# Optimization experiments

Measured on AMD Instinct MI355X. Metric: run time of the kernel, lower is better.

## Reference

```python
import jax, jax.numpy as jnp
import numpy as np

GROUPS = 32
EPS = 1e-5


def conv1x1(x, w, b):
    # x: [B,C,T], w: [O,C], b: [O]
    return jnp.einsum('bct,oc->bot', x, w) + b[None, :, None]


def group_norm(x, g, be):
    B, C, T = x.shape
    xg = x.reshape(B, GROUPS, C // GROUPS, T)
    mean = xg.mean(axis=(2, 3), keepdims=True)
    var = xg.var(axis=(2, 3), keepdims=True)
    xg = (xg - mean) * jax.lax.rsqrt(var + EPS)
    return xg.reshape(B, C, T) * g[None, :, None] + be[None, :, None]


def block(x, w, b, g, be):
    return jax.nn.relu(group_norm(conv1x1(x, w, b), g, be))


def _build_table(x, L):
    # sparse table for range-max: tabs[k][..., t] = max(x[..., t : t+2^k]) (clamped)
    T = x.shape[-1]
    tabs = [x]
    for k in range(1, L + 1):
        step = 1 << (k - 1)
        idx = jnp.minimum(jnp.arange(T) + step, T - 1)
        tabs.append(jnp.maximum(tabs[-1], tabs[-1][..., idx]))
    return jnp.stack(tabs)  # [L+1, B, C, T]


def _range_max_query(S, s, e):
    # S: [L+1,B,C,T]; s,e: [B,N] inclusive range -> [B,C,N]
    length = jnp.maximum(e - s + 1, 1)
    k = jnp.floor(jnp.log2(length.astype(jnp.float32))).astype(jnp.int32)
    e2 = jnp.maximum(e - jnp.left_shift(1, k) + 1, 0)

    def per_b(Sb, kb, sb, eb):
        # Sb: [L+1,C,T]; returns [N,C]
        return jnp.maximum(Sb[kb, :, sb], Sb[kb, :, eb])

    out = jax.vmap(per_b, in_axes=(1, 0, 0, 0))(S, k, s, e2)  # [B,N,C]
    return out.transpose(0, 2, 1)


def boundary_max_pooling(x, segments):
    # x: [B,C,T]; segments: [B,N,4] float boundaries -> [B,C,N]
    B, C, T = x.shape
    s = jnp.clip(jnp.floor(segments).astype(jnp.int32), 0, T - 1)
    e = jnp.clip(jnp.ceil(segments).astype(jnp.int32), 0, T - 1)
    L = max(1, int(np.ceil(np.log2(T))))
    half = C // 2
    S = _build_table(x, L)
    left = _range_max_query(S[:, :, :half], s[..., 0], jnp.maximum(e[..., 1], s[..., 0]))
    right = _range_max_query(S[:, :, half:], s[..., 2], jnp.maximum(e[..., 3], s[..., 2]))
    return jnp.concatenate([left, right], axis=1)


def setup_inputs() -> dict:
    key = jax.random.key(0)
    ks = jax.random.split(key, 12)
    B, Cin, pc, T, Tf, N = 4, 512, 256, 2048, 4096, 2048
    f = lambda k, sh: jax.random.normal(k, sh, jnp.float32)

    def segs(k, tmax):
        raw = jax.random.uniform(k, (B, N, 4), jnp.float32, 0.0, tmax - 1.0)
        return jnp.concatenate([jnp.sort(raw[..., :2], -1), jnp.sort(raw[..., 2:], -1)], -1)

    return {
        'feature': f(ks[0], (B, Cin, T)),
        'frame_level_feature': f(ks[1], (B, pc, Tf)),
        'segments': segs(ks[2], T),
        'frame_segments': segs(ks[3], Tf),
        'feature_lastclass': f(ks[4], (B, 250, N)),
        'ConfResult_feature': f(ks[5], (B, 250, N)),
        'w_cur': f(ks[6], (pc, Cin)) * 0.02, 'b_cur': jnp.zeros((pc,)),
        'g_cur': jnp.ones((pc,)), 'be_cur': jnp.zeros((pc,)),
        'w_lr': f(ks[7], (2 * pc, Cin)) * 0.02, 'b_lr': jnp.zeros((2 * pc,)),
        'g_lr': jnp.ones((2 * pc,)), 'be_lr': jnp.zeros((2 * pc,)),
        'w_roi': f(ks[8], (pc, pc)) * 0.02, 'b_roi': jnp.zeros((pc,)),
        'g_roi': jnp.ones((pc,)), 'be_roi': jnp.zeros((pc,)),
        'w_prop': f(ks[9], (Cin, 4 * pc + 500)) * 0.02, 'b_prop': jnp.zeros((Cin,)),
        'g_prop': jnp.ones((Cin,)), 'be_prop': jnp.zeros((Cin,)),
    }


def reference(feature, frame_level_feature, segments, frame_segments,
              feature_lastclass, ConfResult_feature,
              w_cur, b_cur, g_cur, be_cur,
              w_lr, b_lr, g_lr, be_lr,
              w_roi, b_roi, g_roi, be_roi,
              w_prop, b_prop, g_prop, be_prop):
    fm_short = block(feature, w_cur, b_cur, g_cur, be_cur)          # [B,pc,T]
    feat = block(feature, w_lr, b_lr, g_lr, be_lr)                  # [B,2pc,T]
    prop_feature = boundary_max_pooling(feat, segments)             # [B,2pc,N]
    prop_roi = boundary_max_pooling(frame_level_feature, frame_segments)  # [B,pc,N]
    prop_roi = block(prop_roi, w_roi, b_roi, g_roi, be_roi)
    cat = jnp.concatenate([prop_roi, prop_feature, fm_short,
                           feature_lastclass, ConfResult_feature], axis=1)  # [B,4pc+500,N]
    out = block(cat, w_prop, b_prop, g_prop, be_prop)               # [B,Cin,N]
    return (out, feat)
```

## Files before the change

### kernel.cpp

```cpp
#include <hip/hip_runtime.h>
#include <hip/hip_bf16.h>

#define GROUPS 32
#define EPS_GN 1e-5f

typedef short bf16x8 __attribute__((ext_vector_type(8)));
typedef float f32x4 __attribute__((ext_vector_type(4)));

__device__ __forceinline__ ushort to_bf16_bits(float v) {
  __hip_bfloat16 h = __float2bfloat16(v);
  return *(ushort*)&h;
}
__device__ __forceinline__ float bflo(unsigned u) { return __uint_as_float(u << 16); }
__device__ __forceinline__ float bfhi(unsigned u) { return __uint_as_float(u & 0xffff0000u); }
__device__ __forceinline__ ushort bfpack(float f) {
  return (ushort)(__float_as_uint(f) >> 16);
}

__global__ __launch_bounds__(256)
void cast_w_kernel(const float* __restrict__ w, ushort* __restrict__ wb,
                   int K, int Kp, int total)
{
  int idx = blockIdx.x * 256 + threadIdx.x;
  if (idx >= total) return;
  int o = idx / Kp, k = idx - o * Kp;
  float v = (k < K) ? w[(size_t)o * K + k] : 0.f;
  wb[idx] = to_bf16_bits(v);
}

__global__ __launch_bounds__(256)
void transpose_cast_off(const float* __restrict__ src, ushort* __restrict__ dst,
                        int C, int T, int dstride, int coff, int Cpad)
{
  __shared__ float tile[32][33];
  const int b = blockIdx.z;
  const int c0 = blockIdx.y * 32, t0 = blockIdx.x * 32;
  const int tx = threadIdx.x & 31, ty = threadIdx.x >> 5;
#pragma unroll
  for (int i = 0; i < 4; ++i) {
    const int c = c0 + ty + 8 * i;
    tile[ty + 8 * i][tx] = (c < C) ? src[((size_t)b * C + c) * T + t0 + tx] : 0.f;
  }
  __syncthreads();
  const int cw = c0 + tx;
  if (cw >= Cpad) return;
#pragma unroll
  for (int i = 0; i < 4; ++i)
    dst[((size_t)b * T + t0 + ty + 8 * i) * dstride + coff + cw] =
        to_bf16_bits(tile[tx][ty + 8 * i]);
}

__global__ __launch_bounds__(256)
void bmx_reduce(const ushort* __restrict__ src, ushort* __restrict__ dst,
                int C, int rows, int total8)
{
  int idx = blockIdx.x * 256 + threadIdx.x;
  if (idx >= total8) return;
  const int nc8 = C >> 3;
  const int ci = idx % nc8;
  const int rt = idx / nc8;
  const ushort* p = src + (size_t)rt * rows * C + ci * 8;
  float m[8];
#pragma unroll
  for (int i = 0; i < 8; ++i) m[i] = -3.402823466e38f;
  for (int j = 0; j < rows; ++j) {
    const uint4 v = *(const uint4*)(p + (size_t)j * C);
    m[0] = fmaxf(m[0], bflo(v.x)); m[1] = fmaxf(m[1], bfhi(v.x));
    m[2] = fmaxf(m[2], bflo(v.y)); m[3] = fmaxf(m[3], bfhi(v.y));
    m[4] = fmaxf(m[4], bflo(v.z)); m[5] = fmaxf(m[5], bfhi(v.z));
    m[6] = fmaxf(m[6], bflo(v.w)); m[7] = fmaxf(m[7], bfhi(v.w));
  }
  uint4 o;
  o.x = (unsigned)bfpack(m[0]) | ((unsigned)bfpack(m[1]) << 16);
  o.y = (unsigned)bfpack(m[2]) | ((unsigned)bfpack(m[3]) << 16);
  o.z = (unsigned)bfpack(m[4]) | ((unsigned)bfpack(m[5]) << 16);
  o.w = (unsigned)bfpack(m[6]) | ((unsigned)bfpack(m[7]) << 16);
  *(uint4*)(dst + (size_t)rt * C + ci * 8) = o;
}

template<int CHL>
__global__ __launch_bounds__(256)
void pool_t_kernel(const ushort* __restrict__ xt, const ushort* __restrict__ bx32,
                   const ushort* __restrict__ bx8, const float* __restrict__ segs,
                   ushort* __restrict__ dst,
                   int C, int T, int TB32, int TB8, int N, int dstride, int coff)
{
  const int b    = blockIdx.z;
  const int half = blockIdx.y;
  const int n    = blockIdx.x * 4 + (threadIdx.x >> 6);
  const int lane = threadIdx.x & 63;
  const int c    = half * (C >> 1) + lane * CHL;

  const float4 sg = *(const float4*)(segs + ((size_t)b * N + n) * 4);
  const float f0 = half ? sg.z : sg.x;
  const float f1 = half ? sg.w : sg.y;
  int s = min(max((int)floorf(f0), 0), T - 1);
  int e = min(max((int)ceilf(f1), 0), T - 1);
  e = max(e, s);

  const ushort* xp  = xt  + (size_t)b * T    * C + c;
  const ushort* bp  = bx32+ (size_t)b * TB32 * C + c;
  const ushort* b8p = bx8 + (size_t)b * TB8  * C + c;

  float m[4][CHL];
#pragma unroll
  for (int u = 0; u < 4; ++u)
#pragma unroll
    for (int i = 0; i < CHL; ++i) m[u][i] = -3.402823466e38f;

  auto acc1 = [&](float* mm, const ushort* p) {
    if constexpr (CHL == 4) {
      const uint2 v = *(const uint2*)p;
      mm[0] = fmaxf(mm[0], bflo(v.x)); mm[1] = fmaxf(mm[1], bfhi(v.x));
      mm[2] = fmaxf(mm[2], bflo(v.y)); mm[3] = fmaxf(mm[3], bfhi(v.y));
    } else {
      const unsigned v = *(const unsigned*)p;
      mm[0] = fmaxf(mm[0], bflo(v)); mm[1] = fmaxf(mm[1], bfhi(v));
    }
  };
  auto scan = [&](const ushort* p, int cnt) {
    int i = 0;
    for (; i + 4 <= cnt; i += 4) {
      acc1(m[0], p);
      acc1(m[1], p + (size_t)C);
      acc1(m[2], p + 2 * (size_t)C);
      acc1(m[3], p + 3 * (size_t)C);
      p += 4 * (size_t)C;
    }
    for (; i < cnt; ++i) { acc1(m[0], p); p += (size_t)C; }
  };

  const int b0 = s >> 5, b1 = e >> 5;
  if (b0 == b1) {
    scan(xp + (size_t)s * C, e - s + 1);
  } else {
    const int t0e = (b0 + 1) << 5;
    const int a8 = (s + 7) & ~7;
    scan(xp + (size_t)s * C, a8 - s);
    scan(b8p + (size_t)(a8 >> 3) * C, (t0e - a8) >> 3);
    scan(bp + (size_t)(b0 + 1) * C, b1 - b0 - 1);
    const int r0 = b1 << 5;
    const int cnt8 = ((e + 1) >> 3) - (r0 >> 3);
    scan(b8p + (size_t)(r0 >> 3) * C, cnt8);
    const int ts = r0 + (cnt8 << 3);
    scan(xp + (size_t)ts * C, e - ts + 1);
  }

#pragma unroll
  for (int i = 0; i < CHL; ++i)
    m[0][i] = fmaxf(fmaxf(m[0][i], m[1][i]), fmaxf(m[2][i], m[3][i]));

  ushort* op = dst + ((size_t)b * N + n) * dstride + coff + c;
  if constexpr (CHL == 4) {
    uint2 o;
    o.x = (unsigned)bfpack(m[0][0]) | ((unsigned)bfpack(m[0][1]) << 16);
    o.y = (unsigned)bfpack(m[0][2]) | ((unsigned)bfpack(m[0][3]) << 16);
    *(uint2*)op = o;
  } else {
    *(unsigned*)op = (unsigned)bfpack(m[0][0]) | ((unsigned)bfpack(m[0][1]) << 16);
  }
}

__global__ __launch_bounds__(256)
void mfma_gemm(const ushort* __restrict__ Wb, const ushort* __restrict__ Xt,
               const float* __restrict__ bias, float* __restrict__ out,
               int O, int K, int T)
{
  const int b  = blockIdx.z;
  const int o0 = blockIdx.y * 128;
  const int t0 = blockIdx.x * 128;
  const int lane = threadIdx.x & 63;
  const int wid  = threadIdx.x >> 6;
  const int wm = wid >> 1, wn = wid & 1;
  const int lr = lane & 15;
  const int lq = lane >> 4;

  const ushort* wp = Wb + (size_t)(o0 + wm * 64 + lr) * K + lq * 8;
  const ushort* xp = Xt + ((size_t)b * T + t0 + wn * 64 + lr) * K + lq * 8;

  f32x4 acc[4][4];
#pragma unroll
  for (int i = 0; i < 4; ++i)
#pragma unroll
    for (int j = 0; j < 4; ++j) acc[i][j] = (f32x4){0.f, 0.f, 0.f, 0.f};

  for (int k0 = 0; k0 < K; k0 += 32) {
    bf16x8 a[4], bt[4];
#pragma unroll
    for (int i = 0; i < 4; ++i)
      a[i] = *(const bf16x8*)(wp + (size_t)i * 16 * K + k0);
#pragma unroll
    for (int j = 0; j < 4; ++j)
      bt[j] = *(const bf16x8*)(xp + (size_t)j * 16 * K + k0);
#pragma unroll
    for (int i = 0; i < 4; ++i)
#pragma unroll
      for (int j = 0; j < 4; ++j)
        acc[i][j] = __builtin_amdgcn_mfma_f32_16x16x32_bf16(a[i], bt[j], acc[i][j], 0, 0, 0);
  }

#pragma unroll
  for (int i = 0; i < 4; ++i) {
#pragma unroll
    for (int r = 0; r < 4; ++r) {
      const int o = o0 + wm * 64 + i * 16 + lq * 4 + r;
      const float bs = bias[o];
      float* op = out + ((size_t)b * O + o) * T + t0 + wn * 64 + lr;
#pragma unroll
      for (int j = 0; j < 4; ++j) op[j * 16] = acc[i][j][r] + bs;
    }
  }
}

__global__ __launch_bounds__(256)
void gn_relu_inplace(float* __restrict__ x, const float* __restrict__ gamma,
                     const float* __restrict__ beta, int C, int Tn, int tshift)
{
  const int b = blockIdx.x / GROUPS;
  const int g = blockIdx.x % GROUPS;
  const int Cg = C / GROUPS;
  const size_t base = ((size_t)b * C + (size_t)g * Cg) * Tn;
  const int M = Cg * Tn;
  const int tid = threadIdx.x;

  float sum = 0.f, ss = 0.f;
  for (int i = tid * 4; i < M; i += 256 * 4) {
    float4 v = *(const float4*)(x + base + i);
    sum += v.x + v.y + v.z + v.w;
    ss  += v.x * v.x + v.y * v.y + v.z * v.z + v.w * v.w;
  }
#pragma unroll
  for (int off = 32; off > 0; off >>= 1) {
    sum += __shfl_down(sum, off);
    ss  += __shfl_down(ss, off);
  }
  __shared__ float s1[4], s2[4];
  __shared__ float smean, sinv;
  const int wid = tid >> 6, lane = tid & 63;
  if (lane == 0) { s1[wid] = sum; s2[wid] = ss; }
  __syncthreads();
  if (tid == 0) {
    float t1 = s1[0] + s1[1] + s1[2] + s1[3];
    float t2 = s2[0] + s2[1] + s2[2] + s2[3];
    float mean = t1 / (float)M;
    float var  = t2 / (float)M - mean * mean;
    smean = mean;
    sinv  = rsqrtf(var + EPS_GN);
  }
  __syncthreads();
  const float mean = smean, inv = sinv;
  for (int i = tid * 4; i < M; i += 256 * 4) {
    float4 v = *(const float4*)(x + base + i);
    const int ch = g * Cg + (i >> tshift);
    const float sc = gamma[ch] * inv;
    const float sh = beta[ch] - mean * sc;
    v.x = fmaxf(v.x * sc + sh, 0.f);
    v.y = fmaxf(v.y * sc + sh, 0.f);
    v.z = fmaxf(v.z * sc + sh, 0.f);
    v.w = fmaxf(v.w * sc + sh, 0.f);
    *(float4*)(x + base + i) = v;
  }
}

extern "C" void kernel_launch(void* const* d_in, const int* in_sizes, int n_in,
                              void* d_out, int out_size, void* d_ws, size_t ws_size,
                              hipStream_t stream)
{
  (void)in_sizes; (void)n_in; (void)out_size; (void)ws_size;

  const float* feature  = (const float*)d_in[0];
  const float* frame    = (const float*)d_in[1];
  const float* segments = (const float*)d_in[2];
  const float* fsegs    = (const float*)d_in[3];
  const float* flc      = (const float*)d_in[4];
  const float* conf     = (const float*)d_in[5];
  const float* w_cur  = (const float*)d_in[6];
  const float* b_cur  = (const float*)d_in[7];
  const float* g_cur  = (const float*)d_in[8];
  const float* be_cur = (const float*)d_in[9];
  const float* w_lr   = (const float*)d_in[10];
  const float* b_lr   = (const float*)d_in[11];
  const float* g_lr   = (const float*)d_in[12];
  const float* be_lr  = (const float*)d_in[13];
  const float* w_roi  = (const float*)d_in[14];
  const float* b_roi  = (const float*)d_in[15];
  const float* g_roi  = (const float*)d_in[16];
  const float* be_roi = (const float*)d_in[17];
  const float* w_prop = (const float*)d_in[18];
  const float* b_prop = (const float*)d_in[19];
  const float* g_prop = (const float*)d_in[20];
  const float* be_prop= (const float*)d_in[21];

  float* OUT0 = (float*)d_out;
  float* FOUT = (float*)d_out + 4194304;

  float* ws  = (float*)d_ws;
  float* Y1  = ws;
  float* RF  = Y1 + 2097152;
  ushort* U    = (ushort*)(RF + 2097152);
  ushort* FT   = U;
  ushort* FRT  = FT + 4194304;
  ushort* BX8F = FRT + 4194304;
  ushort* BX32F= BX8F + 524288;
  ushort* BX8R = BX32F + 131072;
  ushort* BX32R= BX8R + 524288;
  ushort* RPT  = BX32R + 131072;
  ushort* CATT = RPT + 2097152;
  ushort* WCB  = CATT + 12582912;
  ushort* WLB  = WCB + 131072;
  ushort* WRB  = WLB + 262144;
  ushort* WPB  = WRB + 65536;

  cast_w_kernel<<<dim3(512),  256, 0, stream>>>(w_cur,  WCB, 512, 512, 131072);
  cast_w_kernel<<<dim3(1024), 256, 0, stream>>>(w_lr,   WLB, 512, 512, 262144);
  cast_w_kernel<<<dim3(256),  256, 0, stream>>>(w_roi,  WRB, 256, 256, 65536);
  cast_w_kernel<<<dim3(3072), 256, 0, stream>>>(w_prop, WPB, 1524, 1536, 786432);

  transpose_cast_off<<<dim3(64, 16, 4), 256, 0, stream>>>(feature, FT, 512, 2048, 512, 0, 512);

  mfma_gemm<<<dim3(16, 2, 4), 256, 0, stream>>>(WCB, FT, b_cur, Y1, 256, 512, 2048);
  gn_relu_inplace<<<dim3(128), 256, 0, stream>>>(Y1, g_cur, be_cur, 256, 2048, 11);

  mfma_gemm<<<dim3(16, 4, 4), 256, 0, stream>>>(WLB, FT, b_lr, FOUT, 512, 512, 2048);
  gn_relu_inplace<<<dim3(128), 256, 0, stream>>>(FOUT, g_lr, be_lr, 512, 2048, 11);

  transpose_cast_off<<<dim3(64, 16, 4), 256, 0, stream>>>(FOUT, FT, 512, 2048, 512, 0, 512);
  bmx_reduce<<<dim3(256), 256, 0, stream>>>(FT,   BX8F,  512, 8, 65536);
  bmx_reduce<<<dim3(64),  256, 0, stream>>>(BX8F, BX32F, 512, 4, 16384);
  pool_t_kernel<4><<<dim3(512, 2, 4), 256, 0, stream>>>(
      FT, BX32F, BX8F, segments, CATT, 512, 2048, 64, 256, 2048, 1536, 256);

  transpose_cast_off<<<dim3(128, 8, 4), 256, 0, stream>>>(frame, FRT, 256, 4096, 256, 0, 256);
  bmx_reduce<<<dim3(256), 256, 0, stream>>>(FRT,  BX8R,  256, 8, 65536);
  bmx_reduce<<<dim3(64),  256, 0, stream>>>(BX8R, BX32R, 256, 4, 16384);
  pool_t_kernel<2><<<dim3(512, 2, 4), 256, 0, stream>>>(
      FRT, BX32R, BX8R, fsegs, RPT, 256, 4096, 128, 512, 2048, 256, 0);

  mfma_gemm<<<dim3(16, 2, 4), 256, 0, stream>>>(WRB, RPT, b_roi, RF, 256, 256, 2048);
  gn_relu_inplace<<<dim3(128), 256, 0, stream>>>(RF, g_roi, be_roi, 256, 2048, 11);

  transpose_cast_off<<<dim3(64, 8, 4), 256, 0, stream>>>(RF,  CATT, 256, 2048, 1536, 0,    256);
  transpose_cast_off<<<dim3(64, 8, 4), 256, 0, stream>>>(Y1,  CATT, 256, 2048, 1536, 768,  256);
  transpose_cast_off<<<dim3(64, 8, 4), 256, 0, stream>>>(flc, CATT, 250, 2048, 1536, 1024, 250);
  transpose_cast_off<<<dim3(64, 9, 4), 256, 0, stream>>>(conf,CATT, 250, 2048, 1536, 1274, 262);

  mfma_gemm<<<dim3(16, 4, 4), 256, 0, stream>>>(WPB, CATT, b_prop, OUT0, 512, 1536, 2048);
  gn_relu_inplace<<<dim3(128), 256, 0, stream>>>(OUT0, g_prop, be_prop, 512, 2048, 11);
}
```

Measured before the change: 413.7 us.

## Stage GEMM tiles through XOR-swizzled LDS with register prefetch

The bf16 MFMA GEMM now loads each 128x64 K-slab of W and X once per block, using coalesced 16-byte global loads, into shared memory with an XOR swizzle. Previously each wave fetched its own fragments straight from global memory, so the same operands were read redundantly across waves. The next slab is prefetched into registers while the current slab is consumed. The cost is two __syncthreads per K step, 32KB of LDS per block, and a requirement that K be a multiple of 64.

```diff
diff --git a/kernel.cpp b/kernel.cpp
--- a/kernel.cpp
+++ b/kernel.cpp
@@ -166,17 +166,27 @@
                const float* __restrict__ bias, float* __restrict__ out,
                int O, int K, int T)
 {
+  __shared__ ushort Al[128 * 64];
+  __shared__ ushort Bl[128 * 64];
+
   const int b  = blockIdx.z;
   const int o0 = blockIdx.y * 128;
   const int t0 = blockIdx.x * 128;
-  const int lane = threadIdx.x & 63;
-  const int wid  = threadIdx.x >> 6;
+  const int tid  = threadIdx.x;
+  const int lane = tid & 63;
+  const int wid  = tid >> 6;
   const int wm = wid >> 1, wn = wid & 1;
   const int lr = lane & 15;
   const int lq = lane >> 4;
 
-  const ushort* wp = Wb + (size_t)(o0 + wm * 64 + lr) * K + lq * 8;
-  const ushort* xp = Xt + ((size_t)b * T + t0 + wn * 64 + lr) * K + lq * 8;
+  const int srow  = tid >> 3;
+  const int sslot = tid & 7;
+  const int wslot = sslot ^ (srow & 7);
+
+  const ushort* wsrc = Wb + (size_t)(o0 + srow) * K + sslot * 8;
+  const ushort* xsrc = Xt + ((size_t)b * T + t0 + srow) * K + sslot * 8;
+  ushort* aw = Al + srow * 64 + wslot * 8;
+  ushort* bw = Bl + srow * 64 + wslot * 8;
 
   f32x4 acc[4][4];
 #pragma unroll
@@ -184,19 +194,47 @@
 #pragma unroll
     for (int j = 0; j < 4; ++j) acc[i][j] = (f32x4){0.f, 0.f, 0.f, 0.f};
 
-  for (int k0 = 0; k0 < K; k0 += 32) {
-    bf16x8 a[4], bt[4];
-#pragma unroll
-    for (int i = 0; i < 4; ++i)
-      a[i] = *(const bf16x8*)(wp + (size_t)i * 16 * K + k0);
-#pragma unroll
-    for (int j = 0; j < 4; ++j)
-      bt[j] = *(const bf16x8*)(xp + (size_t)j * 16 * K + k0);
-#pragma unroll
-    for (int i = 0; i < 4; ++i)
+  uint4 ra[4], rb[4];
+#pragma unroll
+  for (int i = 0; i < 4; ++i) {
+    ra[i] = *(const uint4*)(wsrc + (size_t)i * 32 * K);
+    rb[i] = *(const uint4*)(xsrc + (size_t)i * 32 * K);
+  }
+
+  const int fs0 = (0 * 4 + lq) ^ (lr & 7);
+  const int fs1 = (1 * 4 + lq) ^ (lr & 7);
+
+  for (int k0 = 0; k0 < K; k0 += 64) {
+    __syncthreads();
+#pragma unroll
+    for (int i = 0; i < 4; ++i) {
+      *(uint4*)(aw + i * 32 * 64) = ra[i];
+      *(uint4*)(bw + i * 32 * 64) = rb[i];
+    }
+    __syncthreads();
+    if (k0 + 64 < K) {
+#pragma unroll
+      for (int i = 0; i < 4; ++i) {
+        ra[i] = *(const uint4*)(wsrc + (size_t)i * 32 * K + k0 + 64);
+        rb[i] = *(const uint4*)(xsrc + (size_t)i * 32 * K + k0 + 64);
+      }
+    }
+#pragma unroll
+    for (int h = 0; h < 2; ++h) {
+      const int fs = h ? fs1 : fs0;
+      bf16x8 a[4], bt[4];
+#pragma unroll
+      for (int i = 0; i < 4; ++i)
+        a[i] = *(const bf16x8*)(Al + (wm * 64 + i * 16 + lr) * 64 + fs * 8);
 #pragma unroll
       for (int j = 0; j < 4; ++j)
-        acc[i][j] = __builtin_amdgcn_mfma_f32_16x16x32_bf16(a[i], bt[j], acc[i][j], 0, 0, 0);
+        bt[j] = *(const bf16x8*)(Bl + (wn * 64 + j * 16 + lr) * 64 + fs * 8);
+#pragma unroll
+      for (int i = 0; i < 4; ++i)
+#pragma unroll
+        for (int j = 0; j < 4; ++j)
+          acc[i][j] = __builtin_amdgcn_mfma_f32_16x16x32_bf16(a[i], bt[j], acc[i][j], 0, 0, 0);
+    }
   }
 
 #pragma unroll
```

Measured after the change: 457.3 us. 1.11x slower.
